# Kernel optimization log

Measured on AMD Instinct MI355X. Metric: run time of the kernel, lower is better.

## Reference

```python
import jax, jax.numpy as jnp
import numpy as np

DT = 10.0 / 200  # 0.05
DX = 20.0 / 128  # 0.15625

# 5x5 fixed finite-difference stencils (torch Conv2d = cross-correlation, so use as-is)
_LAPL = np.array([[0, 0, -1/12, 0, 0],
                  [0, 0,  4/3,  0, 0],
                  [-1/12, 4/3, -5, 4/3, -1/12],
                  [0, 0,  4/3,  0, 0],
                  [0, 0, -1/12, 0, 0]], dtype=np.float32)
_PAR_X = np.array([[0, 0,  1/12, 0, 0],
                   [0, 0, -8/12, 0, 0],
                   [0, 0,  0,    0, 0],
                   [0, 0,  8/12, 0, 0],
                   [0, 0, -1/12, 0, 0]], dtype=np.float32)


def _conv2d_valid(x, kern):
    # x: [N, 1, H, W], kern: [5, 5] -> [N, 1, H-4, W-4]
    return jax.lax.conv_general_dilated(x, jnp.asarray(kern)[None, None], (1, 1), 'VALID')


def _time_deriv(x):
    # x: [T, B, 1, h, w]; central diff interior, one-sided at endpoints (all /DT)
    interior = (x[2:] - x[:-2]) / (2.0 * DT)
    t0 = (-1.5 * x[0] + 2.0 * x[1] - 0.5 * x[2]) / DT
    tn = (0.5 * x[-3] - 2.0 * x[-2] + 1.5 * x[-1]) / DT
    return jnp.concatenate([t0[None], interior, tn[None]], axis=0)


def setup_inputs() -> dict:
    key = jax.random.key(0)
    output = jax.random.normal(key, (20, 8, 3, 256, 256), dtype=jnp.float32)
    return {"output": output}


def reference(output):
    T, B, C, H, W = output.shape
    u = output[:, :, 1:2]  # [T,B,1,H,W]
    v = output[:, :, 2:3]

    lap_u = _conv2d_valid(u.reshape(T * B, 1, H, W), _LAPL).reshape(T, B, 1, H - 4, W - 4) / (DX ** 2)
    lap_v = _conv2d_valid(v.reshape(T * B, 1, H, W), _LAPL).reshape(T, B, 1, H - 4, W - 4) / (DX ** 2)

    uc = u[:, :, :, 2:-2, 2:-2]  # [T,B,1,H-4,W-4]
    vc = v[:, :, :, 2:-2, 2:-2]
    u_t = _time_deriv(uc)
    v_t = _time_deriv(vc)

    Du, Dv = 0.16, 0.08
    f, k = 0.06, 0.062
    f_u = Du * lap_u - uc * vc ** 2 + f * (1.0 - uc) - u_t
    f_v = Dv * lap_v + uc * vc ** 2 - (f + k) * vc - v_t
    return (f_u, f_v)
```

## Files before the change

### kernel.cpp

```cpp
#include <hip/hip_runtime.h>


#define T_OUT (8 * 252 * 252)

#define GS_INT(c) { \
    float ut = (ucn.c - u_cm1.c) * hdt; \
    float vt = (vcn.c - v_cm1.c) * hdt; \
    float uvv = u_cc.c * v_cc.c * v_cc.c; \
    fu.c = Du * u_lm1.c - uvv + fR * (1.0f - u_cc.c) - ut; \
    fv.c = Dv * v_lm1.c + uvv - (fR + kR) * v_cc.c - vt; }

#define GS_T0(c) { \
    float ut = (-1.5f * u_cm1.c + 2.0f * u_cc.c - 0.5f * ucn.c) * inv_dt; \
    float vt = (-1.5f * v_cm1.c + 2.0f * v_cc.c - 0.5f * vcn.c) * inv_dt; \
    float uvv = u_cm1.c * v_cm1.c * v_cm1.c; \
    fu.c = Du * u_l0.c - uvv + fR * (1.0f - u_cm1.c) - ut; \
    fv.c = Dv * v_l0.c + uvv - (fR + kR) * v_cm1.c - vt; }

#define GS_TN(c) { \
    float ut = (0.5f * u_cm2.c - 2.0f * u_cm1.c + 1.5f * u_cc.c) * inv_dt; \
    float vt = (0.5f * v_cm2.c - 2.0f * v_cm1.c + 1.5f * v_cc.c) * inv_dt; \
    float uvv = u_cc.c * v_cc.c * v_cc.c; \
    fu.c = Du * u_lm1.c - uvv + fR * (1.0f - u_cc.c) - ut; \
    fv.c = Dv * v_lm1.c + uvv - (fR + kR) * v_cc.c - vt; }

__global__ __launch_bounds__(256) void gs_loss_kernel(
    const float* __restrict__ in, float* __restrict__ out)
{
    const int tid  = threadIdx.x;
    const int xg   = tid & 63;
    const int yloc = tid >> 6;
    if (xg >= 63) return;

    const int bidx  = blockIdx.x;
    const int b     = bidx & 7;
    const int rest  = bidx >> 3;
    const int ytile = rest % 63;
    const int h     = rest / 63;

    const int y  = ytile * 4 + yloc;
    const int x0 = xg * 4;

    const int planeStride = 256 * 256;
    const int bStride     = 3 * planeStride;
    const int tStride     = 8 * bStride;

    const float* ubase = in + (size_t)b * bStride + planeStride
                         + (size_t)(y + 2) * 256 + x0;

    const int total = 20 * T_OUT;
    float* outu = out + ((size_t)b * 252 + y) * 252 + x0;
    float* outv = outu + total;

    const float C1 = 4.0f / 3.0f, C2 = 1.0f / 12.0f;
    const float inv_dx2 = 1.0f / (0.15625f * 0.15625f);
    const float inv_dt  = 20.0f;
    const float hdt     = 10.0f;
    const float Du = 0.16f, Dv = 0.08f, fR = 0.06f, kR = 0.062f;

    float4 u_cm2{}, u_cm1{}, u_cc{}, u_lm1{}, u_l0{};
    float4 v_cm2{}, v_cm1{}, v_cc{}, v_lm1{}, v_l0{};

    const int t_begin = h ? 9 : 0;

    for (int i = 0; i <= 10; ++i) {
        const int t = t_begin + i;
        const float* up = ubase + (size_t)t * tStride;
        const float* vp = up + planeStride;

        float4 uL = *(const float4*)(up);
        float4 uR = *(const float4*)(up + 4);
        float2 um1a = *(const float2*)(up - 256 + 2), um1b = *(const float2*)(up - 256 + 4);
        float2 up1a = *(const float2*)(up + 256 + 2), up1b = *(const float2*)(up + 256 + 4);
        float2 um2a = *(const float2*)(up - 512 + 2), um2b = *(const float2*)(up - 512 + 4);
        float2 up2a = *(const float2*)(up + 512 + 2), up2b = *(const float2*)(up + 512 + 4);

        float4 vL = *(const float4*)(vp);
        float4 vR = *(const float4*)(vp + 4);
        float2 vm1a = *(const float2*)(vp - 256 + 2), vm1b = *(const float2*)(vp - 256 + 4);
        float2 vp1a = *(const float2*)(vp + 256 + 2), vp1b = *(const float2*)(vp + 256 + 4);
        float2 vm2a = *(const float2*)(vp - 512 + 2), vm2b = *(const float2*)(vp - 512 + 4);
        float2 vp2a = *(const float2*)(vp + 512 + 2), vp2b = *(const float2*)(vp + 512 + 4);

        float4 lu, lv;
        lu.x = (C1*(uL.y + uL.w + um1a.x + up1a.x) - C2*(uL.x + uR.x + um2a.x + up2a.x) - 5.0f*uL.z) * inv_dx2;
        lu.y = (C1*(uL.z + uR.x + um1a.y + up1a.y) - C2*(uL.y + uR.y + um2a.y + up2a.y) - 5.0f*uL.w) * inv_dx2;
        lu.z = (C1*(uL.w + uR.y + um1b.x + up1b.x) - C2*(uL.z + uR.z + um2b.x + up2b.x) - 5.0f*uR.x) * inv_dx2;
        lu.w = (C1*(uR.x + uR.z + um1b.y + up1b.y) - C2*(uL.w + uR.w + um2b.y + up2b.y) - 5.0f*uR.y) * inv_dx2;
        lv.x = (C1*(vL.y + vL.w + vm1a.x + vp1a.x) - C2*(vL.x + vR.x + vm2a.x + vp2a.x) - 5.0f*vL.z) * inv_dx2;
        lv.y = (C1*(vL.z + vR.x + vm1a.y + vp1a.y) - C2*(vL.y + vR.y + vm2a.y + vp2a.y) - 5.0f*vL.w) * inv_dx2;
        lv.z = (C1*(vL.w + vR.y + vm1b.x + vp1b.x) - C2*(vL.z + vR.z + vm2b.x + vp2b.x) - 5.0f*vR.x) * inv_dx2;
        lv.w = (C1*(vR.x + vR.z + vm1b.y + vp1b.y) - C2*(vL.w + vR.w + vm2b.y + vp2b.y) - 5.0f*vR.y) * inv_dx2;

        float4 ucn = make_float4(uL.z, uL.w, uR.x, uR.y);
        float4 vcn = make_float4(vL.z, vL.w, vR.x, vR.y);

        if (h == 0 && i == 0) { u_l0 = lu; v_l0 = lv; }

        if (h == 0 && i == 2) {
            float4 fu, fv;
            GS_T0(x); GS_T0(y); GS_T0(z); GS_T0(w);
            *(float4*)(outu) = fu;
            *(float4*)(outv) = fv;
        }

        if (i >= 2) {
            float4 fu, fv;
            GS_INT(x); GS_INT(y); GS_INT(z); GS_INT(w);
            *(float4*)(outu + (size_t)(t - 1) * T_OUT) = fu;
            *(float4*)(outv + (size_t)(t - 1) * T_OUT) = fv;
        }

        u_cm2 = u_cm1; u_cm1 = u_cc; u_cc = ucn; u_lm1 = lu;
        v_cm2 = v_cm1; v_cm1 = v_cc; v_cc = vcn; v_lm1 = lv;
    }

    if (h == 1) {
        float4 fu, fv;
        GS_TN(x); GS_TN(y); GS_TN(z); GS_TN(w);
        *(float4*)(outu + (size_t)19 * T_OUT) = fu;
        *(float4*)(outv + (size_t)19 * T_OUT) = fv;
    }
}

extern "C" void kernel_launch(void* const* d_in, const int* in_sizes, int n_in,
                              void* d_out, int out_size, void* d_ws, size_t ws_size,
                              hipStream_t stream) {
    const float* in = (const float*)d_in[0];
    float* out = (float*)d_out;

    const int blocks = 8 * 63 * 2;
    gs_loss_kernel<<<blocks, 256, 0, stream>>>(in, out);
}
```

Before: 201.8 us.

## Merge time halves into one block, use nontemporal stores and wider unaligned loads

Each block now walks all 20 time steps instead of splitting time into two halves, which removes the two overlapping frames that both halves recomputed but halves the grid to 504 blocks. Output stores become nontemporal to avoid polluting cache, and the pairs of float2 neighbor loads are merged into single unaligned 16-byte loads. The smaller grid may underfill the GPU's compute units and lengthen each block's serial chain, offsetting the saved redundant reads.

```diff
diff --git a/kernel.cpp b/kernel.cpp
--- a/kernel.cpp
+++ b/kernel.cpp
@@ -2,6 +2,14 @@
 
 
 #define T_OUT (8 * 252 * 252)
+
+typedef float vf4 __attribute__((ext_vector_type(4)));
+
+static __device__ __forceinline__ vf4 ldu4(const float* p) {
+    vf4 v;
+    __builtin_memcpy(&v, p, 16);
+    return v;
+}
 
 #define GS_INT(c) { \
     float ut = (ucn.c - u_cm1.c) * hdt; \
@@ -32,11 +40,8 @@
     const int yloc = tid >> 6;
     if (xg >= 63) return;
 
-    const int bidx  = blockIdx.x;
-    const int b     = bidx & 7;
-    const int rest  = bidx >> 3;
-    const int ytile = rest % 63;
-    const int h     = rest / 63;
+    const int b     = blockIdx.x & 7;
+    const int ytile = blockIdx.x >> 3;
 
     const int y  = ytile * 4 + yloc;
     const int x0 = xg * 4;
@@ -58,68 +63,65 @@
     const float hdt     = 10.0f;
     const float Du = 0.16f, Dv = 0.08f, fR = 0.06f, kR = 0.062f;
 
-    float4 u_cm2{}, u_cm1{}, u_cc{}, u_lm1{}, u_l0{};
-    float4 v_cm2{}, v_cm1{}, v_cc{}, v_lm1{}, v_l0{};
+    vf4 u_cm2{}, u_cm1{}, u_cc{}, u_lm1{}, u_l0{};
+    vf4 v_cm2{}, v_cm1{}, v_cc{}, v_lm1{}, v_l0{};
 
-    const int t_begin = h ? 9 : 0;
-
-    for (int i = 0; i <= 10; ++i) {
-        const int t = t_begin + i;
+    for (int t = 0; t < 20; ++t) {
         const float* up = ubase + (size_t)t * tStride;
         const float* vp = up + planeStride;
 
-        float4 uL = *(const float4*)(up);
-        float4 uR = *(const float4*)(up + 4);
-        float2 um1a = *(const float2*)(up - 256 + 2), um1b = *(const float2*)(up - 256 + 4);
-        float2 up1a = *(const float2*)(up + 256 + 2), up1b = *(const float2*)(up + 256 + 4);
-        float2 um2a = *(const float2*)(up - 512 + 2), um2b = *(const float2*)(up - 512 + 4);
-        float2 up2a = *(const float2*)(up + 512 + 2), up2b = *(const float2*)(up + 512 + 4);
+        vf4 uL = *(const vf4*)(up);
+        vf4 uR = *(const vf4*)(up + 4);
+        vf4 um1 = ldu4(up - 256 + 2);
+        vf4 up1 = ldu4(up + 256 + 2);
+        vf4 um2 = ldu4(up - 512 + 2);
+        vf4 up2 = ldu4(up + 512 + 2);
 
-        float4 vL = *(const float4*)(vp);
-        float4 vR = *(const float4*)(vp + 4);
-        float2 vm1a = *(const float2*)(vp - 256 + 2), vm1b = *(const float2*)(vp - 256 + 4);
-        float2 vp1a = *(const float2*)(vp + 256 + 2), vp1b = *(const float2*)(vp + 256 + 4);
-        float2 vm2a = *(const float2*)(vp - 512 + 2), vm2b = *(const float2*)(vp - 512 + 4);
-        float2 vp2a = *(const float2*)(vp + 512 + 2), vp2b = *(const float2*)(vp + 512 + 4);
+        vf4 vL = *(const vf4*)(vp);
+        vf4 vR = *(const vf4*)(vp + 4);
+        vf4 vm1 = ldu4(vp - 256 + 2);
+        vf4 vp1 = ldu4(vp + 256 + 2);
+        vf4 vm2 = ldu4(vp - 512 + 2);
+        vf4 vp2 = ldu4(vp + 512 + 2);
 
-        float4 lu, lv;
-        lu.x = (C1*(uL.y + uL.w + um1a.x + up1a.x) - C2*(uL.x + uR.x + um2a.x + up2a.x) - 5.0f*uL.z) * inv_dx2;
-        lu.y = (C1*(uL.z + uR.x + um1a.y + up1a.y) - C2*(uL.y + uR.y + um2a.y + up2a.y) - 5.0f*uL.w) * inv_dx2;
-        lu.z = (C1*(uL.w + uR.y + um1b.x + up1b.x) - C2*(uL.z + uR.z + um2b.x + up2b.x) - 5.0f*uR.x) * inv_dx2;
-        lu.w = (C1*(uR.x + uR.z + um1b.y + up1b.y) - C2*(uL.w + uR.w + um2b.y + up2b.y) - 5.0f*uR.y) * inv_dx2;
-        lv.x = (C1*(vL.y + vL.w + vm1a.x + vp1a.x) - C2*(vL.x + vR.x + vm2a.x + vp2a.x) - 5.0f*vL.z) * inv_dx2;
-        lv.y = (C1*(vL.z + vR.x + vm1a.y + vp1a.y) - C2*(vL.y + vR.y + vm2a.y + vp2a.y) - 5.0f*vL.w) * inv_dx2;
-        lv.z = (C1*(vL.w + vR.y + vm1b.x + vp1b.x) - C2*(vL.z + vR.z + vm2b.x + vp2b.x) - 5.0f*vR.x) * inv_dx2;
-        lv.w = (C1*(vR.x + vR.z + vm1b.y + vp1b.y) - C2*(vL.w + vR.w + vm2b.y + vp2b.y) - 5.0f*vR.y) * inv_dx2;
+        vf4 lu, lv;
+        lu.x = (C1*(uL.y + uL.w + um1.x + up1.x) - C2*(uL.x + uR.x + um2.x + up2.x) - 5.0f*uL.z) * inv_dx2;
+        lu.y = (C1*(uL.z + uR.x + um1.y + up1.y) - C2*(uL.y + uR.y + um2.y + up2.y) - 5.0f*uL.w) * inv_dx2;
+        lu.z = (C1*(uL.w + uR.y + um1.z + up1.z) - C2*(uL.z + uR.z + um2.z + up2.z) - 5.0f*uR.x) * inv_dx2;
+        lu.w = (C1*(uR.x + uR.z + um1.w + up1.w) - C2*(uL.w + uR.w + um2.w + up2.w) - 5.0f*uR.y) * inv_dx2;
+        lv.x = (C1*(vL.y + vL.w + vm1.x + vp1.x) - C2*(vL.x + vR.x + vm2.x + vp2.x) - 5.0f*vL.z) * inv_dx2;
+        lv.y = (C1*(vL.z + vR.x + vm1.y + vp1.y) - C2*(vL.y + vR.y + vm2.y + vp2.y) - 5.0f*vL.w) * inv_dx2;
+        lv.z = (C1*(vL.w + vR.y + vm1.z + vp1.z) - C2*(vL.z + vR.z + vm2.z + vp2.z) - 5.0f*vR.x) * inv_dx2;
+        lv.w = (C1*(vR.x + vR.z + vm1.w + vp1.w) - C2*(vL.w + vR.w + vm2.w + vp2.w) - 5.0f*vR.y) * inv_dx2;
 
-        float4 ucn = make_float4(uL.z, uL.w, uR.x, uR.y);
-        float4 vcn = make_float4(vL.z, vL.w, vR.x, vR.y);
+        vf4 ucn = {uL.z, uL.w, uR.x, uR.y};
+        vf4 vcn = {vL.z, vL.w, vR.x, vR.y};
 
-        if (h == 0 && i == 0) { u_l0 = lu; v_l0 = lv; }
+        if (t == 0) { u_l0 = lu; v_l0 = lv; }
 
-        if (h == 0 && i == 2) {
-            float4 fu, fv;
+        if (t == 2) {
+            vf4 fu, fv;
             GS_T0(x); GS_T0(y); GS_T0(z); GS_T0(w);
-            *(float4*)(outu) = fu;
-            *(float4*)(outv) = fv;
+            __builtin_nontemporal_store(fu, (vf4*)(outu));
+            __builtin_nontemporal_store(fv, (vf4*)(outv));
         }
 
-        if (i >= 2) {
-            float4 fu, fv;
+        if (t >= 2) {
+            vf4 fu, fv;
             GS_INT(x); GS_INT(y); GS_INT(z); GS_INT(w);
-            *(float4*)(outu + (size_t)(t - 1) * T_OUT) = fu;
-            *(float4*)(outv + (size_t)(t - 1) * T_OUT) = fv;
+            __builtin_nontemporal_store(fu, (vf4*)(outu + (size_t)(t - 1) * T_OUT));
+            __builtin_nontemporal_store(fv, (vf4*)(outv + (size_t)(t - 1) * T_OUT));
         }
 
         u_cm2 = u_cm1; u_cm1 = u_cc; u_cc = ucn; u_lm1 = lu;
         v_cm2 = v_cm1; v_cm1 = v_cc; v_cc = vcn; v_lm1 = lv;
     }
 
-    if (h == 1) {
-        float4 fu, fv;
+    {
+        vf4 fu, fv;
         GS_TN(x); GS_TN(y); GS_TN(z); GS_TN(w);
-        *(float4*)(outu + (size_t)19 * T_OUT) = fu;
-        *(float4*)(outv + (size_t)19 * T_OUT) = fv;
+        __builtin_nontemporal_store(fu, (vf4*)(outu + (size_t)19 * T_OUT));
+        __builtin_nontemporal_store(fv, (vf4*)(outv + (size_t)19 * T_OUT));
     }
 }
 
@@ -129,6 +131,5 @@
     const float* in = (const float*)d_in[0];
     float* out = (float*)d_out;
 
-    const int blocks = 8 * 63 * 2;
-    gs_loss_kernel<<<blocks, 256, 0, stream>>>(in, out);
+    gs_loss_kernel<<<8 * 63, 256, 0, stream>>>(in, out);
 }
```

Result: faster. 196.9 us (-2.4%).
